# Kernel optimization log

Measured on AMD Instinct MI355X. Metric: run time of the kernel, lower is better.

## Reference

```python
import jax, jax.numpy as jnp
import numpy as np

D = 128; H = 4; HD = 32; K = 4; OUT = 2; COND = 6; FF = 256

def _ln(x, g, b):
    m = x.mean(-1, keepdims=True)
    v = ((x - m) ** 2).mean(-1, keepdims=True)
    return g * (x - m) * jax.lax.rsqrt(v + 1e-5) + b

def setup_inputs() -> dict:
    key = jax.random.key(0)
    ks = jax.random.split(key, 40)
    B, S = 4096, 128
    def w(k, shape, scale=0.05):
        return (jax.random.normal(k, shape, dtype=jnp.float32) * scale)
    inp = {
        'x': jax.random.normal(ks[0], (B, OUT, S), dtype=jnp.float32),
        'timesteps': jax.random.randint(ks[1], (B,), 0, 1000, dtype=jnp.int32),
        'conditions': jax.random.normal(ks[2], (B, S, COND), dtype=jnp.float32),
        # time embedding MLP: Linear(128->256), SiLU, Linear(256->128)
        't_w1': w(ks[3], (D, 2 * D)), 't_b1': jnp.zeros((2 * D,), jnp.float32),
        't_w2': w(ks[4], (2 * D, D)), 't_b2': jnp.zeros((D,), jnp.float32),
        # condition MLP: Linear(6->64), SiLU, Linear(64->128), SiLU
        'c_w1': w(ks[5], (COND, D // 2)), 'c_b1': jnp.zeros((D // 2,), jnp.float32),
        'c_w2': w(ks[6], (D // 2, D)), 'c_b2': jnp.zeros((D,), jnp.float32),
        # 2 transformer encoder layers (post-norm, relu FFN, dropout=0 eval)
        'attn_wqkv': w(ks[7], (2, D, 3 * D)), 'attn_bqkv': jnp.zeros((2, 3 * D), jnp.float32),
        'attn_wo': w(ks[8], (2, D, D)), 'attn_bo': jnp.zeros((2, D), jnp.float32),
        'ln1_g': jnp.ones((2, D), jnp.float32), 'ln1_b': jnp.zeros((2, D), jnp.float32),
        'ff_w1': w(ks[9], (2, D, FF)), 'ff_b1': jnp.zeros((2, FF), jnp.float32),
        'ff_w2': w(ks[10], (2, FF, D)), 'ff_b2': jnp.zeros((2, D), jnp.float32),
        'ln2_g': jnp.ones((2, D), jnp.float32), 'ln2_b': jnp.zeros((2, D), jnp.float32),
        # mixture weights net: Linear(256->128), SiLU, Linear(128->4), Softmax
        'mw_w1': w(ks[11], (2 * D, D)), 'mw_b1': jnp.zeros((D,), jnp.float32),
        'mw_w2': w(ks[12], (D, K)), 'mw_b2': jnp.zeros((K,), jnp.float32),
        # K student networks: Linear(2+256->128), Tanh, Linear(128->2)
        's_w1': w(ks[13], (K, OUT + 2 * D, D)), 's_b1': jnp.zeros((K, D), jnp.float32),
        's_w2': w(ks[14], (K, D, OUT)), 's_b2': jnp.zeros((K, OUT), jnp.float32),
    }
    return inp

def reference(x, timesteps, conditions, t_w1, t_b1, t_w2, t_b2, c_w1, c_b1, c_w2, c_b2,
              attn_wqkv, attn_bqkv, attn_wo, attn_bo, ln1_g, ln1_b, ff_w1, ff_b1,
              ff_w2, ff_b2, ln2_g, ln2_b, mw_w1, mw_b1, mw_w2, mw_b2,
              s_w1, s_b1, s_w2, s_b2):
    B, _, S = x.shape
    # sinusoidal time embedding
    half = D // 2
    freqs = jnp.exp(-jnp.log(jnp.float32(10000.0)) * jnp.arange(half, dtype=jnp.float32) / half)
    args = timesteps.astype(jnp.float32)[:, None] * freqs[None, :]
    te = jnp.concatenate([jnp.cos(args), jnp.sin(args)], axis=-1)            # [B, D]
    time_emb = jax.nn.silu(te @ t_w1 + t_b1) @ t_w2 + t_b2                   # [B, D]
    # condition embedding MLP
    h = jax.nn.silu(conditions @ c_w1 + c_b1)
    h = jax.nn.silu(h @ c_w2 + c_b2)                                          # [B, S, D]
    # 2-layer transformer encoder (post-norm)
    for l in range(2):
        qkv = h @ attn_wqkv[l] + attn_bqkv[l]                                 # [B, S, 3D]
        q, k, v = jnp.split(qkv, 3, axis=-1)
        q = q.reshape(B, S, H, HD); k = k.reshape(B, S, H, HD); v = v.reshape(B, S, H, HD)
        sc = jnp.einsum('bqhd,bkhd->bhqk', q, k) / jnp.sqrt(jnp.float32(HD))
        a = jax.nn.softmax(sc, axis=-1)
        o = jnp.einsum('bhqk,bkhd->bqhd', a, v).reshape(B, S, D)
        o = o @ attn_wo[l] + attn_bo[l]
        h = _ln(h + o, ln1_g[l], ln1_b[l])
        f = jax.nn.relu(h @ ff_w1[l] + ff_b1[l]) @ ff_w2[l] + ff_b2[l]
        h = _ln(h + f, ln2_g[l], ln2_b[l])
    cond_emb = h.mean(axis=1)                                                 # [B, D]
    combined = jnp.concatenate([time_emb, cond_emb], axis=-1)                 # [B, 2D]
    mw = jax.nn.softmax(jax.nn.silu(combined @ mw_w1 + mw_b1) @ mw_w2 + mw_b2, axis=-1)  # [B, K]
    # students over all seq positions (vectorized over original seq loop)
    xt = jnp.transpose(x, (0, 2, 1))                                          # [B, S, OUT]
    emb_bs = jnp.broadcast_to(combined[:, None, :], (B, S, 2 * D))
    inp = jnp.concatenate([xt, emb_bs], axis=-1)                              # [B, S, OUT+2D]
    hk = jnp.tanh(jnp.einsum('bsi,kio->bsko', inp, s_w1) + s_b1)              # [B, S, K, D]
    ok = jnp.einsum('bsko,koj->bskj', hk, s_w2) + s_b2                        # [B, S, K, OUT]
    out = jnp.einsum('bskj,bk->bsj', ok, mw)                                  # [B, S, OUT]
    return jnp.transpose(out, (0, 2, 1))                                      # [B, OUT, S]
```

## Files before the change

### kernel.cpp

```cpp
#include <hip/hip_runtime.h>

typedef _Float16 hf;
typedef _Float16 hf2 __attribute__((ext_vector_type(2)));
typedef _Float16 hf4 __attribute__((ext_vector_type(4)));
typedef _Float16 hf8 __attribute__((ext_vector_type(8)));
typedef float f4 __attribute__((ext_vector_type(4)));

#define NTH 512
#define ACT_OFF 0
#define P_OFF   32768
#define SC_OFF  40960
#define SMEM_BYTES 73728

#define WSH_QKV 0
#define WSH_WO  98304
#define WSH_FW1 131072
#define WSH_FW2 196608
#define WSH_CW2 262144
#define WSH_TOTAL 270336
#define CEMB_BYTE_OFF 540672
#define SP1_BYTE_OFF  2637824
#define TPH_SW1 0
#define TPH_TW1 131072
#define TPH_TW2 163840
#define TPH_MW1 196608
#define TPH_TOTAL 229376

__device__ __forceinline__ float dsilu(float x){ return x / (1.f + __expf(-x)); }
__device__ __forceinline__ float dtanh(float x){
  float xc = fminf(fmaxf(x, -10.f), 10.f);
  float e = __expf(2.f * xc);
  return (e - 1.f) / (e + 1.f);
}
__device__ __forceinline__ float fdot2f(hf2 a, hf2 b, float c){
#if __has_builtin(__builtin_amdgcn_fdot2)
  return __builtin_amdgcn_fdot2(a, b, c, false);
#else
  return c + (float)a[0]*(float)b[0] + (float)a[1]*(float)b[1];
#endif
}

__global__ void prep_pack(const float* __restrict__ wqkv, const float* __restrict__ wo,
                          const float* __restrict__ fw1, const float* __restrict__ fw2,
                          const float* __restrict__ cw2, hf* __restrict__ ws){
  int idx = blockIdx.x * 256 + threadIdx.x;
  if (idx >= WSH_TOTAL) return;
  float v;
  if (idx < WSH_WO){
    int u = idx; int lh = u / 12288; int l = lh >> 2, h = lh & 3;
    int r = u % 12288; int tl = r >> 9; int lane = (r >> 3) & 63; int j = r & 7;
    int q = lane >> 4, c = lane & 15;
    int tn = tl >> 2, tk = tl & 3;
    int k = tk*32 + q*8 + j, nloc = tn*16 + c;
    int gcol = (nloc >> 5)*128 + h*32 + (nloc & 31);
    v = wqkv[l*49152 + k*384 + gcol];
  } else if (idx < WSH_FW1){
    int u = idx - WSH_WO; int l = u >> 14; int r = u & 16383;
    int tl = r >> 9; int lane = (r >> 3) & 63; int j = r & 7;
    int q = lane >> 4, c = lane & 15;
    int tn = tl >> 2, tk = tl & 3;
    v = wo[l*16384 + (tk*32 + q*8 + j)*128 + tn*16 + c];
  } else if (idx < WSH_FW2){
    int u = idx - WSH_FW1; int lch = u >> 14; int l = lch >> 1, ch = lch & 1; int r = u & 16383;
    int tl = r >> 9; int lane = (r >> 3) & 63; int j = r & 7;
    int q = lane >> 4, c = lane & 15;
    int tn = tl >> 2, tk = tl & 3;
    v = fw1[l*32768 + (tk*32 + q*8 + j)*256 + ch*128 + tn*16 + c];
  } else if (idx < WSH_CW2){
    int u = idx - WSH_FW2; int lch = u >> 14; int l = lch >> 1, ch = lch & 1; int r = u & 16383;
    int tl = r >> 9; int lane = (r >> 3) & 63; int j = r & 7;
    int q = lane >> 4, c = lane & 15;
    int tn = tl >> 2, tk = tl & 3;
    v = fw2[l*32768 + (ch*128 + tk*32 + q*8 + j)*128 + tn*16 + c];
  } else {
    int u = idx - WSH_CW2;
    int tl = u >> 9; int lane = (u >> 3) & 63; int j = u & 7;
    int q = lane >> 4, c = lane & 15;
    int tn = tl >> 1, tk = tl & 1;
    v = cw2[(tk*32 + q*8 + j)*128 + tn*16 + c];
  }
  ws[idx] = (hf)v;
}

__global__ void prep_pack2(const float* __restrict__ s_w1, const float* __restrict__ t_w1,
                           const float* __restrict__ t_w2, const float* __restrict__ mw_w1,
                           hf* __restrict__ sp1){
  int idx = blockIdx.x * 256 + threadIdx.x;
  if (idx >= TPH_TOTAL) return;
  float v;
  if (idx < TPH_TW1){
    int par = idx & 1, j = (idx >> 1) & 127, ip = (idx >> 8) & 127, k = idx >> 15;
    v = s_w1[k*33024 + (2 + 2*ip + par)*128 + j];
  } else if (idx < TPH_TW2){
    int u = idx - TPH_TW1;
    int par = u & 1, tc = (u >> 1) & 255, ip = u >> 9;
    v = t_w1[(2*ip + par)*256 + tc];
  } else if (idx < TPH_MW1){
    int u = idx - TPH_TW2;
    int par = u & 1, j = (u >> 1) & 127, ip = u >> 8;
    v = t_w2[(2*ip + par)*128 + j];
  } else {
    int u = idx - TPH_MW1;
    int par = u & 1, j = (u >> 1) & 127, ip = u >> 8;
    v = mw_w1[(2*ip + par)*128 + j];
  }
  sp1[idx] = (hf)v;
}

template<int KT>
__device__ __forceinline__ void loadA2(hf8 (&ar)[2][KT], const hf* __restrict__ Ag, int npair, int lane){
#pragma unroll
  for (int jn = 0; jn < 2; ++jn)
#pragma unroll
    for (int tk = 0; tk < KT; ++tk)
      ar[jn][tk] = *(const hf8*)(Ag + (((2*npair + jn)*KT + tk) << 9) + lane*8);
}

template<int KT>
__device__ __forceinline__ void gemmBpre(f4 (&acc)[4][2], const hf8 (&ar)[2][KT], const hf* Bh,
                                         int shalf, int lane){
#pragma unroll
  for (int tk = 0; tk < KT; ++tk){
#pragma unroll
    for (int si = 0; si < 4; ++si){
      hf8 b = *(const hf8*)(Bh + (((shalf*4 + si)*KT + tk) << 9) + lane*8);
      acc[si][0] = __builtin_amdgcn_mfma_f32_16x16x32_f16(ar[0][tk], b, acc[si][0], 0, 0, 0);
      acc[si][1] = __builtin_amdgcn_mfma_f32_16x16x32_f16(ar[1][tk], b, acc[si][1], 0, 0, 0);
    }
  }
}

__device__ __forceinline__ void store_packed_b64(hf* dst, int KtilesOut, int ts, int ft,
                                                 f4 v, int q, int c){
  int tk = ft >> 1;
  int qp = ((ft & 1) << 1) + (q >> 1);
  int j0 = (q & 1) << 2;
  hf4 h; h[0] = (hf)v[0]; h[1] = (hf)v[1]; h[2] = (hf)v[2]; h[3] = (hf)v[3];
  *(hf4*)(dst + ((ts*KtilesOut + tk) << 9) + ((qp*16 + c) << 3) + j0) = h;
}

__device__ __forceinline__ void ln_pass(hf* A, const hf* Dh, const float* __restrict__ g,
                                        const float* __restrict__ bb, int t){
  int s = t >> 2, p = t & 3;
  float xr[4][8];
  int offs[4];
  float sum = 0.f, sq = 0.f;
#pragma unroll
  for (int tk = 0; tk < 4; ++tk){
    int off = (((s >> 4) * 4 + tk) << 9) + ((p * 16 + (s & 15)) << 3);
    offs[tk] = off;
    hf8 va = *(const hf8*)(A + off);
    hf8 vd = *(const hf8*)(Dh + off);
#pragma unroll
    for (int j = 0; j < 8; ++j){
      float x = (float)va[j] + (float)vd[j];
      xr[tk][j] = x; sum += x; sq += x * x;
    }
  }
  sum += __shfl_xor(sum, 1); sq += __shfl_xor(sq, 1);
  sum += __shfl_xor(sum, 2); sq += __shfl_xor(sq, 2);
  float mean = sum * (1.f/128.f);
  float rstd = rsqrtf(sq * (1.f/128.f) - mean*mean + 1e-5f);
#pragma unroll
  for (int tk = 0; tk < 4; ++tk){
    int f0 = tk*32 + p*8;
    f4 g0 = *(const f4*)(g + f0); f4 g1 = *(const f4*)(g + f0 + 4);
    f4 b0 = *(const f4*)(bb + f0); f4 b1 = *(const f4*)(bb + f0 + 4);
    hf8 y;
#pragma unroll
    for (int j = 0; j < 4; ++j){
      y[j]     = (hf)((xr[tk][j]     - mean) * rstd * g0[j] + b0[j]);
      y[j + 4] = (hf)((xr[tk][j + 4] - mean) * rstd * g1[j] + b1[j]);
    }
    *(hf8*)(A + offs[tk]) = y;
  }
}

__global__ __launch_bounds__(NTH, 4) void fused_fp(
    const float* __restrict__ cond,
    const float* __restrict__ c_w1, const float* __restrict__ c_b1, const float* __restrict__ c_b2,
    const float* __restrict__ bqkv_g, const float* __restrict__ bo_g,
    const float* __restrict__ ln1g_g, const float* __restrict__ ln1b_g,
    const float* __restrict__ fb1_g, const float* __restrict__ fb2_g,
    const float* __restrict__ ln2g_g, const float* __restrict__ ln2b_g,
    const hf* __restrict__ wsp, float* __restrict__ cemb)
{
  extern __shared__ char smem[];
  hf* ACTh = (hf*)(smem + ACT_OFF);
  hf* Ph   = (hf*)(smem + P_OFF);
  hf* SCh  = (hf*)(smem + SC_OFF);
  float* SCf = (float*)(smem + SC_OFF);
  hf* Qh  = SCh;
  hf* Kh  = (hf*)(smem + SC_OFF + 8192);
  hf* VTh = (hf*)(smem + SC_OFF + 16384);
  float* cst  = SCf + 4096;
  float* cw1s = SCf + 4864;

  const int b = blockIdx.x;
  const int t = threadIdx.x;
  const int w = t >> 6, lane = t & 63, q = lane >> 4, c = lane & 15;
  const int sp = w & 3, np = w >> 2;
  const int npair = w & 3, shalf = w >> 2;

  for (int idx = t; idx < 768; idx += NTH) cst[idx] = cond[b * 768 + idx];
  if (t < 384) cw1s[t] = c_w1[t];
  if (t < 64)  cw1s[384 + t] = c_b1[t];
  __syncthreads();

  for (int idx = t; idx < 8192; idx += NTH){
    int s = idx >> 6, jf = idx & 63;
    float a = cw1s[384 + jf];
#pragma unroll
    for (int cc = 0; cc < 6; ++cc) a += cst[s * 6 + cc] * cw1s[cc * 64 + jf];
    SCh[(((s >> 4)*2 + (jf >> 5)) << 9) + ((((jf & 31) >> 3)*16 + (s & 15)) << 3) + (jf & 7)] = (hf)dsilu(a);
  }
  {
    hf8 acw[2][2];
    loadA2<2>(acw, wsp + WSH_CW2, npair, lane);
    __syncthreads();
    f4 acc[4][2];
#pragma unroll
    for (int i = 0; i < 4; ++i)
#pragma unroll
      for (int j = 0; j < 2; ++j){ f4 z = {0.f,0.f,0.f,0.f}; acc[i][j] = z; }
    gemmBpre<2>(acc, acw, SCh, shalf, lane);
    f4 cb0 = *(const f4*)(c_b2 + (2*npair    )*16 + q*4);
    f4 cb1 = *(const f4*)(c_b2 + (2*npair + 1)*16 + q*4);
#pragma unroll
    for (int si = 0; si < 4; ++si)
#pragma unroll
      for (int jn = 0; jn < 2; ++jn){
        f4 v = acc[si][jn];
        f4 cb = jn ? cb1 : cb0;
#pragma unroll
        for (int r = 0; r < 4; ++r) v[r] = dsilu(v[r] + cb[r]);
        store_packed_b64(ACTh, 4, shalf*4 + si, 2*npair + jn, v, q, c);
      }
  }

  for (int l = 0; l < 2; ++l){
    f4 oacc[8];
#pragma unroll
    for (int i = 0; i < 8; ++i){ f4 z = {0.f,0.f,0.f,0.f}; oacc[i] = z; }

    for (int h = 0; h < 4; ++h){
      hf8 aq[3][4];
      {
        const hf* Aq = wsp + WSH_QKV + (l*4 + h)*12288;
#pragma unroll
        for (int jn = 0; jn < 3; ++jn)
#pragma unroll
          for (int tk = 0; tk < 4; ++tk)
            aq[jn][tk] = *(const hf8*)(Aq + (((np*3 + jn)*4 + tk) << 9) + lane*8);
      }
      __syncthreads();
      {
        f4 acc[2][3];
#pragma unroll
        for (int i = 0; i < 2; ++i)
#pragma unroll
          for (int j = 0; j < 3; ++j){ f4 z = {0.f,0.f,0.f,0.f}; acc[i][j] = z; }
#pragma unroll
        for (int tk = 0; tk < 4; ++tk){
          hf8 b0 = *(const hf8*)(ACTh + (((2*sp  )*4 + tk) << 9) + lane*8);
          hf8 b1 = *(const hf8*)(ACTh + (((2*sp+1)*4 + tk) << 9) + lane*8);
#pragma unroll
          for (int jn = 0; jn < 3; ++jn){
            acc[0][jn] = __builtin_amdgcn_mfma_f32_16x16x32_f16(aq[jn][tk], b0, acc[0][jn], 0, 0, 0);
            acc[1][jn] = __builtin_amdgcn_mfma_f32_16x16x32_f16(aq[jn][tk], b1, acc[1][jn], 0, 0, 0);
          }
        }
#pragma unroll
        for (int si = 0; si < 2; ++si)
#pragma unroll
          for (int jn = 0; jn < 3; ++jn){
            int ft = np*3 + jn, ts = 2*sp + si;
            int sel = ft >> 1;
            f4 v = acc[si][jn];
            f4 bq = *(const f4*)(bqkv_g + l*384 + sel*128 + h*32 + (ft & 1)*16 + q*4);
#pragma unroll
            for (int r = 0; r < 4; ++r) v[r] += bq[r];
            if (sel == 0){
#pragma unroll
              for (int r = 0; r < 4; ++r) v[r] *= 0.17677669529663687f;
              store_packed_b64(Qh, 1, ts, ft, v, q, c);
            } else if (sel == 1){
              store_packed_b64(Kh, 1, ts, ft - 2, v, q, c);
            } else {
              int td = ft - 4;
              int qp = ((ts & 1) << 1) + (c >> 3);
              hf* pb = VTh + ((td*4 + (ts >> 1)) << 9) + (c & 7);
#pragma unroll
              for (int r = 0; r < 4; ++r) pb[(qp*16 + q*4 + r) << 3] = (hf)v[r];
            }
          }
      }
      __syncthreads();
      {
        hf8 qf = *(const hf8*)(Qh + (w << 9) + lane*8);
        f4 sc[8];
#pragma unroll
        for (int kst = 0; kst < 8; ++kst){
          hf8 kv = *(const hf8*)(Kh + (kst << 9) + lane*8);
          f4 z = {0.f,0.f,0.f,0.f};
          sc[kst] = __builtin_amdgcn_mfma_f32_16x16x32_f16(kv, qf, z, 0, 0, 0);
        }
        float ls = 0.f;
#pragma unroll
        for (int kst = 0; kst < 8; ++kst)
#pragma unroll
          for (int r = 0; r < 4; ++r){
            float e = __expf(sc[kst][r]);
            sc[kst][r] = e; ls += e;
          }
        ls += __shfl_xor(ls, 16);
        ls += __shfl_xor(ls, 32);
        float rl = 1.f / ls;
        hf* Pw = Ph + (w << 9);
#pragma unroll
        for (int ks = 0; ks < 4; ++ks){
#pragma unroll
          for (int h2 = 0; h2 < 2; ++h2){
            int kst = 2*ks + h2;
            int qp = h2*2 + (q >> 1);
            int j0 = (q & 1) << 2;
            hf4 pv;
#pragma unroll
            for (int r = 0; r < 4; ++r) pv[r] = (hf)(sc[kst][r] * rl);
            *(hf4*)(Pw + qp*128 + c*8 + j0) = pv;
          }
          hf8 bp = *(const hf8*)(Pw + lane*8);
          hf8 a0 = *(const hf8*)(VTh + ((     ks) << 9) + lane*8);
          hf8 a1 = *(const hf8*)(VTh + ((4 +  ks) << 9) + lane*8);
          oacc[2*h]     = __builtin_amdgcn_mfma_f32_16x16x32_f16(a0, bp, oacc[2*h],     0, 0, 0);
          oacc[2*h + 1] = __builtin_amdgcn_mfma_f32_16x16x32_f16(a1, bp, oacc[2*h + 1], 0, 0, 0);
        }
      }
    }

    hf8 awo[2][4];
    loadA2<4>(awo, wsp + WSH_WO + l*16384, npair, lane);
    __syncthreads();
#pragma unroll
    for (int ft = 0; ft < 8; ++ft) store_packed_b64(SCh, 4, w, ft, oacc[ft], q, c);
    __syncthreads();

    {
      f4 acc[4][2];
#pragma unroll
      for (int i = 0; i < 4; ++i)
#pragma unroll
        for (int j = 0; j < 2; ++j){ f4 z = {0.f,0.f,0.f,0.f}; acc[i][j] = z; }
      gemmBpre<4>(acc, awo, SCh, shalf, lane);
      __syncthreads();
      f4 bo0 = *(const f4*)(bo_g + l*128 + (2*npair    )*16 + q*4);
      f4 bo1 = *(const f4*)(bo_g + l*128 + (2*npair + 1)*16 + q*4);
#pragma unroll
      for (int si = 0; si < 4; ++si)
#pragma unroll
        for (int jn = 0; jn < 2; ++jn){
          f4 v = acc[si][jn];
          f4 bo = jn ? bo1 : bo0;
#pragma unroll
          for (int r = 0; r < 4; ++r) v[r] += bo[r];
          store_packed_b64(SCh, 4, shalf*4 + si, 2*npair + jn, v, q, c);
        }
    }
    __syncthreads();
    ln_pass(ACTh, SCh, ln1g_g + l*128, ln1b_g + l*128, t);

    {
      f4 facc[4][2];
#pragma unroll
      for (int i = 0; i < 4; ++i)
#pragma unroll
        for (int j = 0; j < 2; ++j){ f4 z = {0.f,0.f,0.f,0.f}; facc[i][j] = z; }
      hf8 af1[2][4], af2[2][4];
      loadA2<4>(af1, wsp + WSH_FW1 + (l*2 + 0)*16384, npair, lane);
      __syncthreads();
      {
        f4 acc[4][2];
#pragma unroll
        for (int i = 0; i < 4; ++i)
#pragma unroll
          for (int j = 0; j < 2; ++j){ f4 z = {0.f,0.f,0.f,0.f}; acc[i][j] = z; }
        gemmBpre<4>(acc, af1, ACTh, shalf, lane);
        f4 fb0 = *(const f4*)(fb1_g + l*256 + (2*npair    )*16 + q*4);
        f4 fb1v = *(const f4*)(fb1_g + l*256 + (2*npair + 1)*16 + q*4);
#pragma unroll
        for (int si = 0; si < 4; ++si)
#pragma unroll
          for (int jn = 0; jn < 2; ++jn){
            f4 v = acc[si][jn];
            f4 fb = jn ? fb1v : fb0;
#pragma unroll
            for (int r = 0; r < 4; ++r) v[r] = fmaxf(v[r] + fb[r], 0.f);
            store_packed_b64(SCh, 4, shalf*4 + si, 2*npair + jn, v, q, c);
          }
      }
      loadA2<4>(af2, wsp + WSH_FW2 + (l*2 + 0)*16384, npair, lane);
      __syncthreads();
      gemmBpre<4>(facc, af2, SCh, shalf, lane);
      loadA2<4>(af1, wsp + WSH_FW1 + (l*2 + 1)*16384, npair, lane);
      __syncthreads();
      {
        f4 acc[4][2];
#pragma unroll
        for (int i = 0; i < 4; ++i)
#pragma unroll
          for (int j = 0; j < 2; ++j){ f4 z = {0.f,0.f,0.f,0.f}; acc[i][j] = z; }
        gemmBpre<4>(acc, af1, ACTh, shalf, lane);
        f4 fb0 = *(const f4*)(fb1_g + l*256 + 128 + (2*npair    )*16 + q*4);
        f4 fb1v = *(const f4*)(fb1_g + l*256 + 128 + (2*npair + 1)*16 + q*4);
#pragma unroll
        for (int si = 0; si < 4; ++si)
#pragma unroll
          for (int jn = 0; jn < 2; ++jn){
            f4 v = acc[si][jn];
            f4 fb = jn ? fb1v : fb0;
#pragma unroll
            for (int r = 0; r < 4; ++r) v[r] = fmaxf(v[r] + fb[r], 0.f);
            store_packed_b64(SCh, 4, shalf*4 + si, 2*npair + jn, v, q, c);
          }
      }
      loadA2<4>(af2, wsp + WSH_FW2 + (l*2 + 1)*16384, npair, lane);
      __syncthreads();
      gemmBpre<4>(facc, af2, SCh, shalf, lane);
      __syncthreads();
      f4 f20 = *(const f4*)(fb2_g + l*128 + (2*npair    )*16 + q*4);
      f4 f21 = *(const f4*)(fb2_g + l*128 + (2*npair + 1)*16 + q*4);
#pragma unroll
      for (int si = 0; si < 4; ++si)
#pragma unroll
        for (int jn = 0; jn < 2; ++jn){
          f4 v = facc[si][jn];
          f4 fb = jn ? f21 : f20;
#pragma unroll
          for (int r = 0; r < 4; ++r) v[r] += fb[r];
          store_packed_b64(SCh, 4, shalf*4 + si, 2*npair + jn, v, q, c);
        }
    }
    __syncthreads();
    ln_pass(ACTh, SCh, ln2g_g + l*128, ln2b_g + l*128, t);
    __syncthreads();
  }

  {
    int o = t & 15;
    float fs[8];
#pragma unroll
    for (int j = 0; j < 8; ++j) fs[j] = 0.f;
#pragma unroll
    for (int u = 0; u < 4; ++u){
      int s = (t >> 4)*4 + u;
      hf8 v = *(const hf8*)(ACTh + (((s >> 4)*4 + (o >> 2)) << 9) + (((o & 3)*16 + (s & 15)) << 3));
#pragma unroll
      for (int j = 0; j < 8; ++j) fs[j] += (float)v[j];
    }
#pragma unroll
    for (int j = 0; j < 8; ++j){
      fs[j] += __shfl_xor(fs[j], 16);
      fs[j] += __shfl_xor(fs[j], 32);
    }
    if (lane < 16){
      f4 v0, v1;
#pragma unroll
      for (int j = 0; j < 4; ++j){ v0[j] = fs[j]; v1[j] = fs[j+4]; }
      *(f4*)(SCf + w*128 + o*8)     = v0;
      *(f4*)(SCf + w*128 + o*8 + 4) = v1;
    }
  }
  __syncthreads();
  if (t < 128){
    float a = 0.f;
#pragma unroll
    for (int wv = 0; wv < 8; ++wv) a += SCf[wv*128 + t];
    cemb[b*128 + t] = a * (1.f/128.f);
  }
}

__global__ __launch_bounds__(256, 8) void tail_k(
    const float* __restrict__ x, const int* __restrict__ tstep, const float* __restrict__ cemb,
    const float* __restrict__ t_b1, const float* __restrict__ t_b2,
    const float* __restrict__ mw_b1,
    const float* __restrict__ mw_w2, const float* __restrict__ mw_b2,
    const float* __restrict__ s_w1, const float* __restrict__ s_b1,
    const float* __restrict__ s_w2, const float* __restrict__ s_b2,
    const hf* __restrict__ sp1, float* __restrict__ out)
{
  __shared__ float sw01[1024], sw2[1024];
  __shared__ float cvec[512];
  __shared__ float scr[1024];
  __shared__ float mwh[128], mwls[4];
  __shared__ hf te_h[128], th_h[256], comb_h[256];
  const int b = blockIdx.x;
  const int t = threadIdx.x;

  for (int i = t; i < 1024; i += 256){
    int row = i >> 9, k = (i >> 7) & 3, j = i & 127;
    sw01[i] = s_w1[k*33024 + row*128 + j];
    sw2[i]  = s_w2[i];
  }
  if (t < 128){
    int i = t & 63;
    float f = __expf(-logf(10000.f) * (float)i * (1.f/64.f));
    float a = (float)tstep[b] * f;
    te_h[t] = (hf)((t < 64) ? cosf(a) : sinf(a));
    comb_h[128 + t] = (hf)cemb[b*128 + t];
  }
  __syncthreads();

  {
    const hf* tp1 = sp1 + TPH_TW1;
    float a = t_b1[t];
#pragma unroll 8
    for (int ii = 0; ii < 64; ++ii){
      hf2 wp = *(const hf2*)(tp1 + ii*512 + 2*t);
      hf2 tp = *(const hf2*)(te_h + 2*ii);
      a = fdot2f(tp, wp, a);
    }
    th_h[t] = (hf)dsilu(a);
  }
  __syncthreads();

  {
    const hf* tp2 = sp1 + TPH_TW2;
    int ih = t >> 7, j = t & 127;
    float a = ih ? 0.f : t_b2[j];
#pragma unroll 8
    for (int ii = 0; ii < 64; ++ii){
      hf2 wp = *(const hf2*)(tp2 + (ih*64 + ii)*256 + 2*j);
      hf2 tp = *(const hf2*)(th_h + ih*128 + 2*ii);
      a = fdot2f(tp, wp, a);
    }
    scr[t] = a;
  }
  __syncthreads();
  if (t < 128) comb_h[t] = (hf)(scr[t] + scr[128 + t]);
  __syncthreads();

  {
    const hf* swp = sp1 + TPH_SW1;
    int ih = t >> 7, k = (t >> 5) & 3, j4 = t & 31;
    f4 a = {0.f, 0.f, 0.f, 0.f};
    const hf* wp = swp + ((k*128 + ih*64)*128 + j4*4)*2;
#pragma unroll 4
    for (int ii = 0; ii < 64; ++ii){
      hf8 wv = *(const hf8*)(wp + ii*256);
      hf2 cb = *(const hf2*)(comb_h + ih*128 + 2*ii);
      hf2 w01; w01[0] = wv[0]; w01[1] = wv[1];
      hf2 w23; w23[0] = wv[2]; w23[1] = wv[3];
      hf2 w45; w45[0] = wv[4]; w45[1] = wv[5];
      hf2 w67; w67[0] = wv[6]; w67[1] = wv[7];
      a[0] = fdot2f(cb, w01, a[0]);
      a[1] = fdot2f(cb, w23, a[1]);
      a[2] = fdot2f(cb, w45, a[2]);
      a[3] = fdot2f(cb, w67, a[3]);
    }
    ((f4*)scr)[ih*128 + k*32 + j4] = a;
  }
  __syncthreads();

  if (t < 128){
    f4 r0 = ((f4*)scr)[t];
    f4 r1 = ((f4*)scr)[128 + t];
    int k = t >> 5, j4 = t & 31;
    f4 sb = *(const f4*)(s_b1 + k*128 + j4*4);
    f4 r; r[0] = r0[0]+r1[0]+sb[0]; r[1] = r0[1]+r1[1]+sb[1];
    r[2] = r0[2]+r1[2]+sb[2]; r[3] = r0[3]+r1[3]+sb[3];
    ((f4*)cvec)[t] = r;
  } else {
    const hf* mp1 = sp1 + TPH_MW1;
    int j = t - 128;
    float a = mw_b1[j];
#pragma unroll 8
    for (int ii = 0; ii < 128; ++ii){
      hf2 wp = *(const hf2*)(mp1 + ii*256 + 2*j);
      hf2 cp = *(const hf2*)(comb_h + 2*ii);
      a = fdot2f(cp, wp, a);
    }
    mwh[j] = dsilu(a);
  }
  __syncthreads();

  if (t < 64){
    int cc = t & 3, j0 = t >> 2;
    float a = 0.f;
#pragma unroll
    for (int i = 0; i < 8; ++i){
      int j = j0 + 16*i;
      a += mwh[j] * mw_w2[j*4 + cc];
    }
    a += __shfl_xor(a, 4);
    a += __shfl_xor(a, 8);
    a += __shfl_xor(a, 16);
    a += __shfl_xor(a, 32);
    if (t < 4) mwls[t] = a + mw_b2[t];
  }
#pragma unroll
  for (int u = 0; u < 2; ++u){
    int o = t + u*256, k = o >> 7, s = o & 127;
    float x0 = x[b*256 + s];
    float x1 = x[b*256 + 128 + s];
    float a0 = 0.f, a1 = 0.f;
    const f4* cvp = (const f4*)cvec + k*32;
    const f4* w0p = (const f4*)sw01 + k*32;
    const f4* w1p = (const f4*)sw01 + 128 + k*32;
    const f4* s2p = (const f4*)sw2 + k*64;
#pragma unroll 2
    for (int j4 = 0; j4 < 32; ++j4){
      f4 cv = cvp[j4], w0 = w0p[j4], w1 = w1p[j4];
      f4 s20 = s2p[2*j4], s21 = s2p[2*j4 + 1];
      float h0 = dtanh(cv[0] + x0*w0[0] + x1*w1[0]);
      float h1 = dtanh(cv[1] + x0*w0[1] + x1*w1[1]);
      float h2 = dtanh(cv[2] + x0*w0[2] + x1*w1[2]);
      float h3 = dtanh(cv[3] + x0*w0[3] + x1*w1[3]);
      a0 += h0*s20[0] + h1*s20[2] + h2*s21[0] + h3*s21[2];
      a1 += h0*s20[1] + h1*s20[3] + h2*s21[1] + h3*s21[3];
    }
    scr[k*256 + s]       = a0 + s_b2[2*k];
    scr[k*256 + 128 + s] = a1 + s_b2[2*k + 1];
  }
  __syncthreads();

  {
    int row = t >> 7, s = t & 127;
    float l0 = mwls[0], l1 = mwls[1], l2 = mwls[2], l3 = mwls[3];
    float mx = fmaxf(fmaxf(l0, l1), fmaxf(l2, l3));
    float e0 = __expf(l0 - mx), e1 = __expf(l1 - mx), e2 = __expf(l2 - mx), e3 = __expf(l3 - mx);
    float rs = 1.f / (e0 + e1 + e2 + e3);
    float a = e0*scr[0*256 + row*128 + s] + e1*scr[1*256 + row*128 + s]
            + e2*scr[2*256 + row*128 + s] + e3*scr[3*256 + row*128 + s];
    out[b*256 + row*128 + s] = a * rs;
  }
}

extern "C" void kernel_launch(void* const* d_in, const int* in_sizes, int n_in,
                              void* d_out, int out_size, void* d_ws, size_t ws_size,
                              hipStream_t stream){
  (void)n_in; (void)ws_size; (void)out_size;
  hipFuncSetAttribute((const void*)fused_fp, hipFuncAttributeMaxDynamicSharedMemorySize, SMEM_BYTES);
  int B = in_sizes[1];
  hf* wsp = (hf*)d_ws;
  float* cemb = (float*)((char*)d_ws + CEMB_BYTE_OFF);
  hf* sp1 = (hf*)((char*)d_ws + SP1_BYTE_OFF);
  prep_pack<<<dim3((WSH_TOTAL + 255) / 256), dim3(256), 0, stream>>>(
      (const float*)d_in[11], (const float*)d_in[13], (const float*)d_in[17],
      (const float*)d_in[19], (const float*)d_in[9], wsp);
  prep_pack2<<<dim3((TPH_TOTAL + 255) / 256), dim3(256), 0, stream>>>(
      (const float*)d_in[27], (const float*)d_in[3], (const float*)d_in[5],
      (const float*)d_in[23], sp1);
  fused_fp<<<dim3(B), dim3(NTH), SMEM_BYTES, stream>>>(
      (const float*)d_in[2],
      (const float*)d_in[7], (const float*)d_in[8], (const float*)d_in[10],
      (const float*)d_in[12], (const float*)d_in[14],
      (const float*)d_in[15], (const float*)d_in[16],
      (const float*)d_in[18], (const float*)d_in[20],
      (const float*)d_in[21], (const float*)d_in[22],
      wsp, cemb);
  tail_k<<<dim3(B), dim3(256), 0, stream>>>(
      (const float*)d_in[0], (const int*)d_in[1], cemb,
      (const float*)d_in[4], (const float*)d_in[6],
      (const float*)d_in[24],
      (const float*)d_in[25], (const float*)d_in[26],
      (const float*)d_in[27], (const float*)d_in[28], (const float*)d_in[29], (const float*)d_in[30],
      sp1, (float*)d_out);
}
```

Measured before the change: 1.053 ms.

## Repartition MFMA GEMM tiling across warps, keeping activations in registers

Changes how the 8 warps split each small GEMM. Weight fragments are now streamed from global memory inside the k-loop and activation fragments are held in registers, instead of prefetching weights into registers and reading activations from LDS. For QKV each warp now owns one 16-row sequence tile and loads the activation fragment once per layer. For the FFN, activations are kept in registers across both hidden chunks. This cuts LDS reads and some barriers, at the cost of more global or L2 weight loads that are no longer prefetched ahead of the sync.

```diff
diff --git a/kernel.cpp b/kernel.cpp
--- a/kernel.cpp
+++ b/kernel.cpp
@@ -108,24 +108,31 @@
 }
 
 template<int KT>
-__device__ __forceinline__ void loadA2(hf8 (&ar)[2][KT], const hf* __restrict__ Ag, int npair, int lane){
-#pragma unroll
-  for (int jn = 0; jn < 2; ++jn)
-#pragma unroll
-    for (int tk = 0; tk < KT; ++tk)
-      ar[jn][tk] = *(const hf8*)(Ag + (((2*npair + jn)*KT + tk) << 9) + lane*8);
+__device__ __forceinline__ void gemmC(f4 (&acc)[2][4], const hf* __restrict__ Ag, const hf* Bh,
+                                      int nq, int sp2, int lane){
+#pragma unroll
+  for (int tk = 0; tk < KT; ++tk){
+    hf8 b0 = *(const hf8*)(Bh + (((sp2*2    )*KT + tk) << 9) + lane*8);
+    hf8 b1 = *(const hf8*)(Bh + (((sp2*2 + 1)*KT + tk) << 9) + lane*8);
+#pragma unroll
+    for (int jn = 0; jn < 4; ++jn){
+      hf8 a = *(const hf8*)(Ag + (((nq*4 + jn)*KT + tk) << 9) + lane*8);
+      acc[0][jn] = __builtin_amdgcn_mfma_f32_16x16x32_f16(a, b0, acc[0][jn], 0, 0, 0);
+      acc[1][jn] = __builtin_amdgcn_mfma_f32_16x16x32_f16(a, b1, acc[1][jn], 0, 0, 0);
+    }
+  }
 }
 
 template<int KT>
-__device__ __forceinline__ void gemmBpre(f4 (&acc)[4][2], const hf8 (&ar)[2][KT], const hf* Bh,
-                                         int shalf, int lane){
+__device__ __forceinline__ void gemmCpreB(f4 (&acc)[2][4], const hf* __restrict__ Ag,
+                                          const hf8 (&br)[2][KT], int nq, int lane){
 #pragma unroll
   for (int tk = 0; tk < KT; ++tk){
 #pragma unroll
-    for (int si = 0; si < 4; ++si){
-      hf8 b = *(const hf8*)(Bh + (((shalf*4 + si)*KT + tk) << 9) + lane*8);
-      acc[si][0] = __builtin_amdgcn_mfma_f32_16x16x32_f16(ar[0][tk], b, acc[si][0], 0, 0, 0);
-      acc[si][1] = __builtin_amdgcn_mfma_f32_16x16x32_f16(ar[1][tk], b, acc[si][1], 0, 0, 0);
+    for (int jn = 0; jn < 4; ++jn){
+      hf8 a = *(const hf8*)(Ag + (((nq*4 + jn)*KT + tk) << 9) + lane*8);
+      acc[0][jn] = __builtin_amdgcn_mfma_f32_16x16x32_f16(a, br[0][tk], acc[0][jn], 0, 0, 0);
+      acc[1][jn] = __builtin_amdgcn_mfma_f32_16x16x32_f16(a, br[1][tk], acc[1][jn], 0, 0, 0);
     }
   }
 }
@@ -199,8 +206,7 @@
   const int b = blockIdx.x;
   const int t = threadIdx.x;
   const int w = t >> 6, lane = t & 63, q = lane >> 4, c = lane & 15;
-  const int sp = w & 3, np = w >> 2;
-  const int npair = w & 3, shalf = w >> 2;
+  const int nq = w & 1, sp2 = w >> 1;
 
   for (int idx = t; idx < 768; idx += NTH) cst[idx] = cond[b * 768 + idx];
   if (t < 384) cw1s[t] = c_w1[t];
@@ -214,86 +220,76 @@
     for (int cc = 0; cc < 6; ++cc) a += cst[s * 6 + cc] * cw1s[cc * 64 + jf];
     SCh[(((s >> 4)*2 + (jf >> 5)) << 9) + ((((jf & 31) >> 3)*16 + (s & 15)) << 3) + (jf & 7)] = (hf)dsilu(a);
   }
+  __syncthreads();
+
   {
-    hf8 acw[2][2];
-    loadA2<2>(acw, wsp + WSH_CW2, npair, lane);
-    __syncthreads();
-    f4 acc[4][2];
-#pragma unroll
-    for (int i = 0; i < 4; ++i)
-#pragma unroll
-      for (int j = 0; j < 2; ++j){ f4 z = {0.f,0.f,0.f,0.f}; acc[i][j] = z; }
-    gemmBpre<2>(acc, acw, SCh, shalf, lane);
-    f4 cb0 = *(const f4*)(c_b2 + (2*npair    )*16 + q*4);
-    f4 cb1 = *(const f4*)(c_b2 + (2*npair + 1)*16 + q*4);
-#pragma unroll
-    for (int si = 0; si < 4; ++si)
-#pragma unroll
-      for (int jn = 0; jn < 2; ++jn){
+    f4 acc[2][4];
+#pragma unroll
+    for (int i = 0; i < 2; ++i)
+#pragma unroll
+      for (int j = 0; j < 4; ++j){ f4 z = {0.f,0.f,0.f,0.f}; acc[i][j] = z; }
+    gemmC<2>(acc, wsp + WSH_CW2, SCh, nq, sp2, lane);
+#pragma unroll
+    for (int jn = 0; jn < 4; ++jn){
+      int ft = nq*4 + jn;
+      f4 cb = *(const f4*)(c_b2 + ft*16 + q*4);
+#pragma unroll
+      for (int si = 0; si < 2; ++si){
         f4 v = acc[si][jn];
-        f4 cb = jn ? cb1 : cb0;
 #pragma unroll
         for (int r = 0; r < 4; ++r) v[r] = dsilu(v[r] + cb[r]);
-        store_packed_b64(ACTh, 4, shalf*4 + si, 2*npair + jn, v, q, c);
+        store_packed_b64(ACTh, 4, sp2*2 + si, ft, v, q, c);
       }
+    }
   }
 
   for (int l = 0; l < 2; ++l){
     f4 oacc[8];
 #pragma unroll
     for (int i = 0; i < 8; ++i){ f4 z = {0.f,0.f,0.f,0.f}; oacc[i] = z; }
+    hf8 bact[4];
 
     for (int h = 0; h < 4; ++h){
-      hf8 aq[3][4];
+      __syncthreads();
+      if (h == 0){
+#pragma unroll
+        for (int tk = 0; tk < 4; ++tk)
+          bact[tk] = *(const hf8*)(ACTh + ((w*4 + tk) << 9) + lane*8);
+      }
       {
         const hf* Aq = wsp + WSH_QKV + (l*4 + h)*12288;
-#pragma unroll
-        for (int jn = 0; jn < 3; ++jn)
-#pragma unroll
-          for (int tk = 0; tk < 4; ++tk)
-            aq[jn][tk] = *(const hf8*)(Aq + (((np*3 + jn)*4 + tk) << 9) + lane*8);
-      }
-      __syncthreads();
-      {
-        f4 acc[2][3];
-#pragma unroll
-        for (int i = 0; i < 2; ++i)
-#pragma unroll
-          for (int j = 0; j < 3; ++j){ f4 z = {0.f,0.f,0.f,0.f}; acc[i][j] = z; }
+        f4 acc[6];
+#pragma unroll
+        for (int i = 0; i < 6; ++i){ f4 z = {0.f,0.f,0.f,0.f}; acc[i] = z; }
 #pragma unroll
         for (int tk = 0; tk < 4; ++tk){
-          hf8 b0 = *(const hf8*)(ACTh + (((2*sp  )*4 + tk) << 9) + lane*8);
-          hf8 b1 = *(const hf8*)(ACTh + (((2*sp+1)*4 + tk) << 9) + lane*8);
-#pragma unroll
-          for (int jn = 0; jn < 3; ++jn){
-            acc[0][jn] = __builtin_amdgcn_mfma_f32_16x16x32_f16(aq[jn][tk], b0, acc[0][jn], 0, 0, 0);
-            acc[1][jn] = __builtin_amdgcn_mfma_f32_16x16x32_f16(aq[jn][tk], b1, acc[1][jn], 0, 0, 0);
+#pragma unroll
+          for (int jn = 0; jn < 6; ++jn){
+            hf8 a = *(const hf8*)(Aq + ((jn*4 + tk) << 9) + lane*8);
+            acc[jn] = __builtin_amdgcn_mfma_f32_16x16x32_f16(a, bact[tk], acc[jn], 0, 0, 0);
           }
         }
 #pragma unroll
-        for (int si = 0; si < 2; ++si)
-#pragma unroll
-          for (int jn = 0; jn < 3; ++jn){
-            int ft = np*3 + jn, ts = 2*sp + si;
-            int sel = ft >> 1;
-            f4 v = acc[si][jn];
-            f4 bq = *(const f4*)(bqkv_g + l*384 + sel*128 + h*32 + (ft & 1)*16 + q*4);
-#pragma unroll
-            for (int r = 0; r < 4; ++r) v[r] += bq[r];
-            if (sel == 0){
-#pragma unroll
-              for (int r = 0; r < 4; ++r) v[r] *= 0.17677669529663687f;
-              store_packed_b64(Qh, 1, ts, ft, v, q, c);
-            } else if (sel == 1){
-              store_packed_b64(Kh, 1, ts, ft - 2, v, q, c);
-            } else {
-              int td = ft - 4;
-              int qp = ((ts & 1) << 1) + (c >> 3);
-              hf* pb = VTh + ((td*4 + (ts >> 1)) << 9) + (c & 7);
-#pragma unroll
-              for (int r = 0; r < 4; ++r) pb[(qp*16 + q*4 + r) << 3] = (hf)v[r];
-            }
+        for (int ft = 0; ft < 6; ++ft){
+          int sel = ft >> 1;
+          f4 v = acc[ft];
+          f4 bq = *(const f4*)(bqkv_g + l*384 + sel*128 + h*32 + (ft & 1)*16 + q*4);
+#pragma unroll
+          for (int r = 0; r < 4; ++r) v[r] += bq[r];
+          if (sel == 0){
+#pragma unroll
+            for (int r = 0; r < 4; ++r) v[r] *= 0.17677669529663687f;
+            store_packed_b64(Qh, 1, w, ft, v, q, c);
+          } else if (sel == 1){
+            store_packed_b64(Kh, 1, w, ft - 2, v, q, c);
+          } else {
+            int td = ft - 4;
+            int qp = ((w & 1) << 1) + (c >> 3);
+            hf* pb = VTh + ((td*4 + (w >> 1)) << 9) + (c & 7);
+#pragma unroll
+            for (int r = 0; r < 4; ++r) pb[(qp*16 + q*4 + r) << 3] = (hf)v[r];
           }
+        }
       }
       __syncthreads();
       {
@@ -338,107 +334,83 @@
       }
     }
 
-    hf8 awo[2][4];
-    loadA2<4>(awo, wsp + WSH_WO + l*16384, npair, lane);
     __syncthreads();
 #pragma unroll
     for (int ft = 0; ft < 8; ++ft) store_packed_b64(SCh, 4, w, ft, oacc[ft], q, c);
     __syncthreads();
 
     {
-      f4 acc[4][2];
-#pragma unroll
-      for (int i = 0; i < 4; ++i)
-#pragma unroll
-        for (int j = 0; j < 2; ++j){ f4 z = {0.f,0.f,0.f,0.f}; acc[i][j] = z; }
-      gemmBpre<4>(acc, awo, SCh, shalf, lane);
+      f4 acc[2][4];
+#pragma unroll
+      for (int i = 0; i < 2; ++i)
+#pragma unroll
+        for (int j = 0; j < 4; ++j){ f4 z = {0.f,0.f,0.f,0.f}; acc[i][j] = z; }
+      gemmC<4>(acc, wsp + WSH_WO + l*16384, SCh, nq, sp2, lane);
       __syncthreads();
-      f4 bo0 = *(const f4*)(bo_g + l*128 + (2*npair    )*16 + q*4);
-      f4 bo1 = *(const f4*)(bo_g + l*128 + (2*npair + 1)*16 + q*4);
-#pragma unroll
-      for (int si = 0; si < 4; ++si)
-#pragma unroll
-        for (int jn = 0; jn < 2; ++jn){
+#pragma unroll
+      for (int jn = 0; jn < 4; ++jn){
+        int ft = nq*4 + jn;
+        f4 bo = *(const f4*)(bo_g + l*128 + ft*16 + q*4);
+#pragma unroll
+        for (int si = 0; si < 2; ++si){
           f4 v = acc[si][jn];
-          f4 bo = jn ? bo1 : bo0;
 #pragma unroll
           for (int r = 0; r < 4; ++r) v[r] += bo[r];
-          store_packed_b64(SCh, 4, shalf*4 + si, 2*npair + jn, v, q, c);
+          store_packed_b64(SCh, 4, sp2*2 + si, ft, v, q, c);
         }
+      }
     }
     __syncthreads();
     ln_pass(ACTh, SCh, ln1g_g + l*128, ln1b_g + l*128, t);
+    __syncthreads();
 
     {
-      f4 facc[4][2];
-#pragma unroll
-      for (int i = 0; i < 4; ++i)
-#pragma unroll
-        for (int j = 0; j < 2; ++j){ f4 z = {0.f,0.f,0.f,0.f}; facc[i][j] = z; }
-      hf8 af1[2][4], af2[2][4];
-      loadA2<4>(af1, wsp + WSH_FW1 + (l*2 + 0)*16384, npair, lane);
-      __syncthreads();
-      {
-        f4 acc[4][2];
-#pragma unroll
-        for (int i = 0; i < 4; ++i)
-#pragma unroll
-          for (int j = 0; j < 2; ++j){ f4 z = {0.f,0.f,0.f,0.f}; acc[i][j] = z; }
-        gemmBpre<4>(acc, af1, ACTh, shalf, lane);
-        f4 fb0 = *(const f4*)(fb1_g + l*256 + (2*npair    )*16 + q*4);
-        f4 fb1v = *(const f4*)(fb1_g + l*256 + (2*npair + 1)*16 + q*4);
-#pragma unroll
-        for (int si = 0; si < 4; ++si)
-#pragma unroll
-          for (int jn = 0; jn < 2; ++jn){
+      hf8 bffn[2][4];
+#pragma unroll
+      for (int si = 0; si < 2; ++si)
+#pragma unroll
+        for (int tk = 0; tk < 4; ++tk)
+          bffn[si][tk] = *(const hf8*)(ACTh + (((sp2*2 + si)*4 + tk) << 9) + lane*8);
+      f4 facc[2][4];
+#pragma unroll
+      for (int i = 0; i < 2; ++i)
+#pragma unroll
+        for (int j = 0; j < 4; ++j){ f4 z = {0.f,0.f,0.f,0.f}; facc[i][j] = z; }
+      for (int ch = 0; ch < 2; ++ch){
+        f4 acc[2][4];
+#pragma unroll
+        for (int i = 0; i < 2; ++i)
+#pragma unroll
+          for (int j = 0; j < 4; ++j){ f4 z = {0.f,0.f,0.f,0.f}; acc[i][j] = z; }
+        gemmCpreB<4>(acc, wsp + WSH_FW1 + (l*2 + ch)*16384, bffn, nq, lane);
+#pragma unroll
+        for (int jn = 0; jn < 4; ++jn){
+          int ft = nq*4 + jn;
+          f4 fb = *(const f4*)(fb1_g + l*256 + ch*128 + ft*16 + q*4);
+#pragma unroll
+          for (int si = 0; si < 2; ++si){
             f4 v = acc[si][jn];
-            f4 fb = jn ? fb1v : fb0;
 #pragma unroll
             for (int r = 0; r < 4; ++r) v[r] = fmaxf(v[r] + fb[r], 0.f);
-            store_packed_b64(SCh, 4, shalf*4 + si, 2*npair + jn, v, q, c);
+            store_packed_b64(SCh, 4, sp2*2 + si, ft, v, q, c);
           }
+        }
+        __syncthreads();
+        gemmC<4>(facc, wsp + WSH_FW2 + (l*2 + ch)*16384, SCh, nq, sp2, lane);
+        __syncthreads();
       }
-      loadA2<4>(af2, wsp + WSH_FW2 + (l*2 + 0)*16384, npair, lane);
-      __syncthreads();
-      gemmBpre<4>(facc, af2, SCh, shalf, lane);
-      loadA2<4>(af1, wsp + WSH_FW1 + (l*2 + 1)*16384, npair, lane);
-      __syncthreads();
-      {
-        f4 acc[4][2];
-#pragma unroll
-        for (int i = 0; i < 4; ++i)
-#pragma unroll
-          for (int j = 0; j < 2; ++j){ f4 z = {0.f,0.f,0.f,0.f}; acc[i][j] = z; }
-        gemmBpre<4>(acc, af1, ACTh, shalf, lane);
-        f4 fb0 = *(const f4*)(fb1_g + l*256 + 128 + (2*npair    )*16 + q*4);
-        f4 fb1v = *(const f4*)(fb1_g + l*256 + 128 + (2*npair + 1)*16 + q*4);
-#pragma unroll
-        for (int si = 0; si < 4; ++si)
-#pragma unroll
-          for (int jn = 0; jn < 2; ++jn){
-            f4 v = acc[si][jn];
-            f4 fb = jn ? fb1v : fb0;
-#pragma unroll
-            for (int r = 0; r < 4; ++r) v[r] = fmaxf(v[r] + fb[r], 0.f);
-            store_packed_b64(SCh, 4, shalf*4 + si, 2*npair + jn, v, q, c);
-          }
+#pragma unroll
+      for (int jn = 0; jn < 4; ++jn){
+        int ft = nq*4 + jn;
+        f4 fb = *(const f4*)(fb2_g + l*128 + ft*16 + q*4);
+#pragma unroll
+        for (int si = 0; si < 2; ++si){
+          f4 v = facc[si][jn];
+#pragma unroll
+          for (int r = 0; r < 4; ++r) v[r] += fb[r];
+          store_packed_b64(SCh, 4, sp2*2 + si, ft, v, q, c);
+        }
       }
-      loadA2<4>(af2, wsp + WSH_FW2 + (l*2 + 1)*16384, npair, lane);
-      __syncthreads();
-      gemmBpre<4>(facc, af2, SCh, shalf, lane);
-      __syncthreads();
-      f4 f20 = *(const f4*)(fb2_g + l*128 + (2*npair    )*16 + q*4);
-      f4 f21 = *(const f4*)(fb2_g + l*128 + (2*npair + 1)*16 + q*4);
-#pragma unroll
-      for (int si = 0; si < 4; ++si)
-#pragma unroll
-        for (int jn = 0; jn < 2; ++jn){
-          f4 v = facc[si][jn];
-          f4 fb = jn ? f21 : f20;
-#pragma unroll
-          for (int r = 0; r < 4; ++r) v[r] += fb[r];
-          store_packed_b64(SCh, 4, shalf*4 + si, 2*npair + jn, v, q, c);
-        }
     }
     __syncthreads();
     ln_pass(ACTh, SCh, ln2g_g + l*128, ln2b_g + l*128, t);
```

Result: slower. 1.292 ms (+22.7%).
